# Kernel tuning notes

Measured on AMD Instinct MI355X. Metric: run time of the kernel, lower is better.

The kernel has to match this reference:

```python
import jax, jax.numpy as jnp
import numpy as np

B, T, WSZ, HS = 32768, 168, 4, 1  # batch, seq (one week of hours), weather dims, HIDDEN_DIM


def _uniform(key, shape, lim):
    return jax.random.uniform(key, shape, jnp.float32, -lim, lim)


def setup_inputs() -> dict:
    key = jax.random.key(0)
    ks = jax.random.split(key, 12)
    stdv = 1.0 / np.sqrt(HS)  # pew_LSTM init: uniform(-1/sqrt(H), 1/sqrt(H))
    xav = np.sqrt(6.0 / (HS + 1))  # xavier_uniform for fc (in=HS, out=1)
    return {
        "input": jax.random.normal(ks[0], (B, T, WSZ + 1), dtype=jnp.float32),
        # pew_LSTM layer 1 (input_sz=1)
        "W1_ih": _uniform(ks[1], (1, 4 * HS), stdv),
        "W1_hh": _uniform(ks[2], (HS, 4 * HS), stdv),
        "W1_wh": _uniform(ks[3], (WSZ, 4 * HS), stdv),
        "b1": _uniform(ks[4], (4 * HS,), stdv),
        # pew_LSTM layer 2 (input_sz=HS)
        "W2_ih": _uniform(ks[5], (HS, 4 * HS), stdv),
        "W2_hh": _uniform(ks[6], (HS, 4 * HS), stdv),
        "W2_wh": _uniform(ks[7], (WSZ, 4 * HS), stdv),
        "b2": _uniform(ks[8], (4 * HS,), stdv),
        # final Linear(HS, 1)
        "fc_w": _uniform(ks[9], (1, HS), xav),
        "fc_b": jnp.zeros((1,), jnp.float32),
    }


def _pew_lstm(x, w, Wih, Whh, Wwh, b):
    """Custom LSTM with per-step weather input added to the gate pre-activations.
    x: [B,T,D_in], w: [B,T,WSZ] -> hidden_seq [B,T,HS], c_T [B,HS]."""
    bs = x.shape[0]
    h0 = jnp.zeros((bs, HS), x.dtype)
    c0 = jnp.zeros((bs, HS), x.dtype)
    # input- and weather-dependent gate terms are time-parallel; precompute once
    g_pre = jnp.einsum('btd,dg->btg', x, Wih) + jnp.einsum('btw,wg->btg', w, Wwh) + b

    def step(carry, gp_t):
        h, c = carry
        gates = gp_t + h @ Whh  # [B, 4*HS]
        i = jax.nn.sigmoid(gates[:, 0 * HS:1 * HS])
        f = jax.nn.sigmoid(gates[:, 1 * HS:2 * HS])
        g = jnp.tanh(gates[:, 2 * HS:3 * HS])
        o = jax.nn.sigmoid(gates[:, 3 * HS:4 * HS])
        c = f * c + i * g
        h = o * jnp.tanh(c)
        return (h, c), h

    (_, cT), hs = jax.lax.scan(step, (h0, c0), jnp.swapaxes(g_pre, 0, 1))
    return jnp.swapaxes(hs, 0, 1), cT  # [B,T,HS], [B,HS]


def reference(input, W1_ih, W1_hh, W1_wh, b1, W2_ih, W2_hh, W2_wh, b2, fc_w, fc_b):
    x_weather = input[:, :, :-1]            # [B,T,4]
    x_input = input[:, :, -1:]              # [B,T,1]
    h1, _ = _pew_lstm(x_input, x_weather, W1_ih, W1_hh, W1_wh, b1)
    h2, _ = _pew_lstm(h1, x_weather, W2_ih, W2_hh, W2_wh, b2)
    out = h2.reshape(-1, HS) @ fc_w.T + fc_b  # [B*T, 1]
    return out.reshape(-1)                    # [B*T]
```

## Files before the change

### kernel.cpp

```cpp
#include <hip/hip_runtime.h>


constexpr int BB  = 32768;
constexpr int TT  = 168;
constexpr int CHS = 8;
constexpr int CHV = CHS * 5 / 4;
constexpr int NCH = TT / CHS;

#define LOG2E 1.44269504088896341f

__device__ __forceinline__ float sigf(float x) {
    float e = __builtin_amdgcn_exp2f(-x * LOG2E);
    return __builtin_amdgcn_rcpf(1.0f + e);
}
__device__ __forceinline__ float tanh_fast(float x) {
    float e = __builtin_amdgcn_exp2f(-x * (2.0f * LOG2E));
    return fmaf(2.0f, __builtin_amdgcn_rcpf(1.0f + e), -1.0f);
}
__device__ __forceinline__ float lane_swap(float x) {
    return __int_as_float(
        __builtin_amdgcn_mov_dpp(__float_as_int(x), 0xB1, 0xF, 0xF, true));
}

__global__ __launch_bounds__(64, 1) void pewlstm_kernel(
    const float* __restrict__ in,
    const float* __restrict__ W1ih, const float* __restrict__ W1hh,
    const float* __restrict__ W1wh, const float* __restrict__ b1,
    const float* __restrict__ W2ih, const float* __restrict__ W2hh,
    const float* __restrict__ W2wh, const float* __restrict__ b2,
    const float* __restrict__ fcw, const float* __restrict__ fcb,
    float* __restrict__ out)
{
    const int tid = blockIdx.x * 64 + threadIdx.x;
    const int b   = tid >> 1;
    const int l2  = tid & 1;
    const float l2f = l2 ? 1.0f : 0.0f;

    const float* Wih = l2 ? W2ih : W1ih;
    const float* Whh = l2 ? W2hh : W1hh;
    const float* Wwh = l2 ? W2wh : W1wh;
    const float* Bv  = l2 ? b2   : b1;

    float wih[4], whh[4], bbv[4], wwh[16];
#pragma unroll
    for (int g = 0; g < 4; ++g) { wih[g] = Wih[g]; whh[g] = Whh[g]; bbv[g] = Bv[g]; }
#pragma unroll
    for (int k = 0; k < 16; ++k) wwh[k] = Wwh[k];
    const float fw = fcw[0], fbv = fcb[0];

    const float4* __restrict__ row =
        reinterpret_cast<const float4*>(in + (size_t)b * (TT * 5));
    float4 pref[CHV];
#pragma unroll
    for (int i = 0; i < CHV; ++i) pref[i] = row[i];

    float h = 0.f, cc = 0.f;
    float h1x = 0.f;
    float xc0 = 0.f, xc1 = 0.f, xc2 = 0.f, xc3 = 0.f;
    float ob[CHS];
    float4* orow = reinterpret_cast<float4*>(out + (size_t)b * TT);

    for (int c = 0; c < NCH; ++c) {
        float cur[CHS * 5];
#pragma unroll
        for (int i = 0; i < CHV; ++i) {
            float4 v = pref[i];
            cur[4 * i + 0] = v.x; cur[4 * i + 1] = v.y;
            cur[4 * i + 2] = v.z; cur[4 * i + 3] = v.w;
        }
        if (c + 1 < NCH) {
            const float4* nrow = row + (c + 1) * CHV;
#pragma unroll
            for (int i = 0; i < CHV; ++i) pref[i] = nrow[i];
        }

        float pre[CHS][4];
#pragma unroll
        for (int s = 0; s < CHS; ++s) {
            const float w0 = l2 ? (s == 0 ? xc0 : cur[(s - 1) * 5 + 0]) : cur[s * 5 + 0];
            const float w1 = l2 ? (s == 0 ? xc1 : cur[(s - 1) * 5 + 1]) : cur[s * 5 + 1];
            const float w2 = l2 ? (s == 0 ? xc2 : cur[(s - 1) * 5 + 2]) : cur[s * 5 + 2];
            const float w3 = l2 ? (s == 0 ? xc3 : cur[(s - 1) * 5 + 3]) : cur[s * 5 + 3];
            const float xi = l2 ? 0.0f : cur[s * 5 + 4];
#pragma unroll
            for (int g = 0; g < 4; ++g) {
                float p = bbv[g];
                p = fmaf(w0, wwh[0 + g], p);
                p = fmaf(w1, wwh[4 + g], p);
                p = fmaf(w2, wwh[8 + g], p);
                p = fmaf(w3, wwh[12 + g], p);
                pre[s][g] = fmaf(xi, wih[g], p);
            }
        }
        xc0 = cur[7 * 5 + 0]; xc1 = cur[7 * 5 + 1];
        xc2 = cur[7 * 5 + 2]; xc3 = cur[7 * 5 + 3];

#pragma unroll
        for (int s = 0; s < CHS; ++s) {
            const float inv = h1x * l2f;
            float ga[4];
#pragma unroll
            for (int g = 0; g < 4; ++g)
                ga[g] = fmaf(h, whh[g], fmaf(inv, wih[g], pre[s][g]));

            const float ig = sigf(ga[0]);
            const float fg = sigf(ga[1]);
            const float gg = tanh_fast(ga[2]);
            const float og = sigf(ga[3]);
            cc = fmaf(fg, cc, ig * gg);
            h  = og * tanh_fast(cc);

            if (s == 0 && c == 0 && l2) { h = 0.f; cc = 0.f; }

            ob[(s + CHS - 1) & (CHS - 1)] = fmaf(h, fw, fbv);

            if (s == 0 && c >= 1 && l2) {
                orow[(c - 1) * 2 + 0] = make_float4(ob[0], ob[1], ob[2], ob[3]);
                orow[(c - 1) * 2 + 1] = make_float4(ob[4], ob[5], ob[6], ob[7]);
            }

            h1x = lane_swap(h);
        }
    }

    {
        float ga[4];
#pragma unroll
        for (int g = 0; g < 4; ++g) {
            float p = bbv[g];
            p = fmaf(xc0, wwh[0 + g], p);
            p = fmaf(xc1, wwh[4 + g], p);
            p = fmaf(xc2, wwh[8 + g], p);
            p = fmaf(xc3, wwh[12 + g], p);
            p = fmaf(h1x, wih[g], p);
            ga[g] = fmaf(h, whh[g], p);
        }
        const float ig = sigf(ga[0]);
        const float fg = sigf(ga[1]);
        const float gg = tanh_fast(ga[2]);
        const float og = sigf(ga[3]);
        cc = fmaf(fg, cc, ig * gg);
        h  = og * tanh_fast(cc);
        ob[7] = fmaf(h, fw, fbv);
        if (l2) {
            orow[(NCH - 1) * 2 + 0] = make_float4(ob[0], ob[1], ob[2], ob[3]);
            orow[(NCH - 1) * 2 + 1] = make_float4(ob[4], ob[5], ob[6], ob[7]);
        }
    }
}

extern "C" void kernel_launch(void* const* d_in, const int* in_sizes, int n_in,
                              void* d_out, int out_size, void* d_ws, size_t ws_size,
                              hipStream_t stream) {
    const float* in   = (const float*)d_in[0];
    const float* W1ih = (const float*)d_in[1];
    const float* W1hh = (const float*)d_in[2];
    const float* W1wh = (const float*)d_in[3];
    const float* b1   = (const float*)d_in[4];
    const float* W2ih = (const float*)d_in[5];
    const float* W2hh = (const float*)d_in[6];
    const float* W2wh = (const float*)d_in[7];
    const float* b2   = (const float*)d_in[8];
    const float* fcw  = (const float*)d_in[9];
    const float* fcb  = (const float*)d_in[10];
    float* out = (float*)d_out;

    pewlstm_kernel<<<(BB * 2) / 64, 64, 0, stream>>>(
        in, W1ih, W1hh, W1wh, b1, W2ih, W2hh, W2wh, b2, fcw, fcb, out);
}
```

Measured before the change: 32.52 us.

## Fold log2 scaling into weights, merge gate divisions, and software-pipeline chunk preactivations

Pre-scales all gate weights and biases by -log2(e), or -2·log2(e) for the cell gate, so each gate needs only a bare exp2. The sigmoid/tanh products are combined algebraically so each step uses two reciprocals instead of six. It also double-buffers the precomputed gate inputs, interleaving the next chunk's weather FMAs with the current chunk's recurrence to hide latency on the serial dependency chain. In exchange it adds clamping to avoid overflow, slightly different rounding, and more register pressure.

```diff
diff --git a/kernel.cpp b/kernel.cpp
--- a/kernel.cpp
+++ b/kernel.cpp
@@ -4,19 +4,13 @@
 constexpr int BB  = 32768;
 constexpr int TT  = 168;
 constexpr int CHS = 8;
-constexpr int CHV = CHS * 5 / 4;
-constexpr int NCH = TT / CHS;
-
-#define LOG2E 1.44269504088896341f
-
-__device__ __forceinline__ float sigf(float x) {
-    float e = __builtin_amdgcn_exp2f(-x * LOG2E);
-    return __builtin_amdgcn_rcpf(1.0f + e);
-}
-__device__ __forceinline__ float tanh_fast(float x) {
-    float e = __builtin_amdgcn_exp2f(-x * (2.0f * LOG2E));
-    return fmaf(2.0f, __builtin_amdgcn_rcpf(1.0f + e), -1.0f);
-}
+constexpr int CHV = 10;
+constexpr int NCH = 21;
+
+#define LOG2E  1.44269504088896341f
+#define NEG2L  (-2.88539008177792681f)
+#define ACLAMP 40.0f
+
 __device__ __forceinline__ float lane_swap(float x) {
     return __int_as_float(
         __builtin_amdgcn_mov_dpp(__float_as_int(x), 0xB1, 0xF, 0xF, true));
@@ -43,108 +37,168 @@
 
     float wih[4], whh[4], bbv[4], wwh[16];
 #pragma unroll
-    for (int g = 0; g < 4; ++g) { wih[g] = Wih[g]; whh[g] = Whh[g]; bbv[g] = Bv[g]; }
-#pragma unroll
-    for (int k = 0; k < 16; ++k) wwh[k] = Wwh[k];
+    for (int g = 0; g < 4; ++g) {
+        const float s = (g == 2) ? NEG2L : -LOG2E;
+        wih[g] = Wih[g] * s; whh[g] = Whh[g] * s; bbv[g] = Bv[g] * s;
+    }
+#pragma unroll
+    for (int k = 0; k < 16; ++k) {
+        const float s = ((k & 3) == 2) ? NEG2L : -LOG2E;
+        wwh[k] = Wwh[k] * s;
+    }
     const float fw = fcw[0], fbv = fcb[0];
 
     const float4* __restrict__ row =
         reinterpret_cast<const float4*>(in + (size_t)b * (TT * 5));
+    float4* orow = reinterpret_cast<float4*>(out + (size_t)b * TT);
+
     float4 pref[CHV];
 #pragma unroll
     for (int i = 0; i < CHV; ++i) pref[i] = row[i];
 
-    float h = 0.f, cc = 0.f;
-    float h1x = 0.f;
+    float h = 0.f, cc = 0.f, h1x = 0.f;
     float xc0 = 0.f, xc1 = 0.f, xc2 = 0.f, xc3 = 0.f;
     float ob[CHS];
-    float4* orow = reinterpret_cast<float4*>(out + (size_t)b * TT);
-
-    for (int c = 0; c < NCH; ++c) {
-        float cur[CHS * 5];
+    float preA[CHS][4], preB[CHS][4];
+    float cur[CHS * 5];
+
+    auto commit = [&]() {
 #pragma unroll
         for (int i = 0; i < CHV; ++i) {
             float4 v = pref[i];
-            cur[4 * i + 0] = v.x; cur[4 * i + 1] = v.y;
-            cur[4 * i + 2] = v.z; cur[4 * i + 3] = v.w;
-        }
-        if (c + 1 < NCH) {
-            const float4* nrow = row + (c + 1) * CHV;
-#pragma unroll
-            for (int i = 0; i < CHV; ++i) pref[i] = nrow[i];
-        }
-
-        float pre[CHS][4];
+            cur[4*i+0] = v.x; cur[4*i+1] = v.y;
+            cur[4*i+2] = v.z; cur[4*i+3] = v.w;
+        }
+    };
+    auto issue = [&](int c2) {
+        const float4* nr = row + c2 * CHV;
+#pragma unroll
+        for (int i = 0; i < CHV; ++i) pref[i] = nr[i];
+    };
+
+    auto run_chunk = [&](float (&pC)[CHS][4], float (&pN)[CHS][4],
+                         int c, bool buildNext) {
+        const bool is0 = (c == 0);
 #pragma unroll
         for (int s = 0; s < CHS; ++s) {
-            const float w0 = l2 ? (s == 0 ? xc0 : cur[(s - 1) * 5 + 0]) : cur[s * 5 + 0];
-            const float w1 = l2 ? (s == 0 ? xc1 : cur[(s - 1) * 5 + 1]) : cur[s * 5 + 1];
-            const float w2 = l2 ? (s == 0 ? xc2 : cur[(s - 1) * 5 + 2]) : cur[s * 5 + 2];
-            const float w3 = l2 ? (s == 0 ? xc3 : cur[(s - 1) * 5 + 3]) : cur[s * 5 + 3];
-            const float xi = l2 ? 0.0f : cur[s * 5 + 4];
-#pragma unroll
-            for (int g = 0; g < 4; ++g) {
-                float p = bbv[g];
-                p = fmaf(w0, wwh[0 + g], p);
-                p = fmaf(w1, wwh[4 + g], p);
-                p = fmaf(w2, wwh[8 + g], p);
-                p = fmaf(w3, wwh[12 + g], p);
-                pre[s][g] = fmaf(xi, wih[g], p);
+            if (buildNext) {
+                const float w0 = l2 ? (s == 0 ? xc0 : cur[(s-1)*5+0]) : cur[s*5+0];
+                const float w1 = l2 ? (s == 0 ? xc1 : cur[(s-1)*5+1]) : cur[s*5+1];
+                const float w2 = l2 ? (s == 0 ? xc2 : cur[(s-1)*5+2]) : cur[s*5+2];
+                const float w3 = l2 ? (s == 0 ? xc3 : cur[(s-1)*5+3]) : cur[s*5+3];
+                const float xi = l2 ? 0.0f : cur[s*5+4];
+#pragma unroll
+                for (int g = 0; g < 4; ++g) {
+                    float p = bbv[g];
+                    p = fmaf(w0, wwh[0  + g], p);
+                    p = fmaf(w1, wwh[4  + g], p);
+                    p = fmaf(w2, wwh[8  + g], p);
+                    p = fmaf(w3, wwh[12 + g], p);
+                    pN[s][g] = fmaf(xi, wih[g], p);
+                }
             }
-        }
-        xc0 = cur[7 * 5 + 0]; xc1 = cur[7 * 5 + 1];
-        xc2 = cur[7 * 5 + 2]; xc3 = cur[7 * 5 + 3];
-
-#pragma unroll
-        for (int s = 0; s < CHS; ++s) {
             const float inv = h1x * l2f;
-            float ga[4];
-#pragma unroll
-            for (int g = 0; g < 4; ++g)
-                ga[g] = fmaf(h, whh[g], fmaf(inv, wih[g], pre[s][g]));
-
-            const float ig = sigf(ga[0]);
-            const float fg = sigf(ga[1]);
-            const float gg = tanh_fast(ga[2]);
-            const float og = sigf(ga[3]);
-            cc = fmaf(fg, cc, ig * gg);
-            h  = og * tanh_fast(cc);
-
-            if (s == 0 && c == 0 && l2) { h = 0.f; cc = 0.f; }
+            float a0 = fmaf(h, whh[0], fmaf(inv, wih[0], pC[s][0]));
+            float a1 = fmaf(h, whh[1], fmaf(inv, wih[1], pC[s][1]));
+            float a2 = fmaf(h, whh[2], fmaf(inv, wih[2], pC[s][2]));
+            float a3 = fmaf(h, whh[3], fmaf(inv, wih[3], pC[s][3]));
+            a0 = fminf(a0, ACLAMP); a1 = fminf(a1, ACLAMP);
+            a2 = fminf(a2, ACLAMP); a3 = fminf(a3, ACLAMP);
+            const float eI = __builtin_amdgcn_exp2f(a0);
+            const float eF = __builtin_amdgcn_exp2f(a1);
+            const float eG = __builtin_amdgcn_exp2f(a2);
+            const float eO = __builtin_amdgcn_exp2f(a3);
+            const float dI = 1.f + eI, dF = 1.f + eF;
+            const float dG = 1.f + eG, dO = 1.f + eO;
+            const float nG = 1.f - eG;
+            const float p   = dI * dG;
+            const float num = fmaf(cc, p, nG * dF);
+            const float den = dF * p;
+            cc = num * __builtin_amdgcn_rcpf(den);
+            const float Cm = fminf(cc * NEG2L, ACLAMP);
+            const float eC = __builtin_amdgcn_exp2f(Cm);
+            const float dC = 1.f + eC, nC = 1.f - eC;
+            h = nC * __builtin_amdgcn_rcpf(dO * dC);
+
+            if (s == 0) { if (is0 && l2) { h = 0.f; cc = 0.f; } }
 
             ob[(s + CHS - 1) & (CHS - 1)] = fmaf(h, fw, fbv);
 
-            if (s == 0 && c >= 1 && l2) {
-                orow[(c - 1) * 2 + 0] = make_float4(ob[0], ob[1], ob[2], ob[3]);
-                orow[(c - 1) * 2 + 1] = make_float4(ob[4], ob[5], ob[6], ob[7]);
+            if (s == 0 && l2 && c >= 1) {
+                orow[(c-1)*2+0] = make_float4(ob[0], ob[1], ob[2], ob[3]);
+                orow[(c-1)*2+1] = make_float4(ob[4], ob[5], ob[6], ob[7]);
             }
 
             h1x = lane_swap(h);
         }
-    }
+        if (buildNext) {
+            xc0 = cur[35]; xc1 = cur[36]; xc2 = cur[37]; xc3 = cur[38];
+        }
+    };
+
+    commit();
+#pragma unroll
+    for (int s = 0; s < CHS; ++s) {
+        const float w0 = l2 ? (s == 0 ? 0.f : cur[(s-1)*5+0]) : cur[s*5+0];
+        const float w1 = l2 ? (s == 0 ? 0.f : cur[(s-1)*5+1]) : cur[s*5+1];
+        const float w2 = l2 ? (s == 0 ? 0.f : cur[(s-1)*5+2]) : cur[s*5+2];
+        const float w3 = l2 ? (s == 0 ? 0.f : cur[(s-1)*5+3]) : cur[s*5+3];
+        const float xi = l2 ? 0.0f : cur[s*5+4];
+#pragma unroll
+        for (int g = 0; g < 4; ++g) {
+            float pp = bbv[g];
+            pp = fmaf(w0, wwh[0  + g], pp);
+            pp = fmaf(w1, wwh[4  + g], pp);
+            pp = fmaf(w2, wwh[8  + g], pp);
+            pp = fmaf(w3, wwh[12 + g], pp);
+            preA[s][g] = fmaf(xi, wih[g], pp);
+        }
+    }
+    xc0 = cur[35]; xc1 = cur[36]; xc2 = cur[37]; xc3 = cur[38];
+    issue(1);
+
+    for (int cp = 0; cp < 10; ++cp) {
+        const int c0 = 2 * cp;
+        commit();
+        if (c0 + 2 < NCH) issue(c0 + 2);
+        run_chunk(preA, preB, c0, true);
+
+        commit();
+        if (c0 + 3 < NCH) issue(c0 + 3);
+        run_chunk(preB, preA, c0 + 1, true);
+    }
+
+    run_chunk(preA, preB, NCH - 1, false);
 
     {
-        float ga[4];
+        float a[4];
 #pragma unroll
         for (int g = 0; g < 4; ++g) {
-            float p = bbv[g];
-            p = fmaf(xc0, wwh[0 + g], p);
-            p = fmaf(xc1, wwh[4 + g], p);
-            p = fmaf(xc2, wwh[8 + g], p);
-            p = fmaf(xc3, wwh[12 + g], p);
-            p = fmaf(h1x, wih[g], p);
-            ga[g] = fmaf(h, whh[g], p);
-        }
-        const float ig = sigf(ga[0]);
-        const float fg = sigf(ga[1]);
-        const float gg = tanh_fast(ga[2]);
-        const float og = sigf(ga[3]);
-        cc = fmaf(fg, cc, ig * gg);
-        h  = og * tanh_fast(cc);
+            float pp = bbv[g];
+            pp = fmaf(xc0, wwh[0  + g], pp);
+            pp = fmaf(xc1, wwh[4  + g], pp);
+            pp = fmaf(xc2, wwh[8  + g], pp);
+            pp = fmaf(xc3, wwh[12 + g], pp);
+            pp = fmaf(h1x, wih[g], pp);
+            a[g] = fminf(fmaf(h, whh[g], pp), ACLAMP);
+        }
+        const float eI = __builtin_amdgcn_exp2f(a[0]);
+        const float eF = __builtin_amdgcn_exp2f(a[1]);
+        const float eG = __builtin_amdgcn_exp2f(a[2]);
+        const float eO = __builtin_amdgcn_exp2f(a[3]);
+        const float dI = 1.f + eI, dF = 1.f + eF;
+        const float dG = 1.f + eG, dO = 1.f + eO;
+        const float nG = 1.f - eG;
+        const float p   = dI * dG;
+        const float num = fmaf(cc, p, nG * dF);
+        cc = num * __builtin_amdgcn_rcpf(dF * p);
+        const float Cm = fminf(cc * NEG2L, ACLAMP);
+        const float eC = __builtin_amdgcn_exp2f(Cm);
+        h = (1.f - eC) * __builtin_amdgcn_rcpf(dO * (1.f + eC));
         ob[7] = fmaf(h, fw, fbv);
         if (l2) {
-            orow[(NCH - 1) * 2 + 0] = make_float4(ob[0], ob[1], ob[2], ob[3]);
-            orow[(NCH - 1) * 2 + 1] = make_float4(ob[4], ob[5], ob[6], ob[7]);
+            orow[(NCH-1)*2+0] = make_float4(ob[0], ob[1], ob[2], ob[3]);
+            orow[(NCH-1)*2+1] = make_float4(ob[4], ob[5], ob[6], ob[7]);
         }
     }
 }
```

Measured after the change: 33.39 us. +2.7%, slower.
